# Performance work log

Measured on AMD Instinct MI355X. Metric: run time of the kernel, lower is better.

Reference implementation:

```python
import jax, jax.numpy as jnp
import numpy as np

N_RBF = 20
CUTOFF = 5.0
LN_EPS = 1e-5


def setup_inputs() -> dict:
    key = jax.random.key(0)
    ks = jax.random.split(key, 16)
    N, E, F, H = 20000, 160000, 128, 4
    HF = H * F

    def lin_w(k, fin, fout):
        return (jax.random.normal(k, (fin, fout), jnp.float32) / np.sqrt(fin)).astype(jnp.float32)

    inp = {
        "s_j": jax.random.normal(ks[0], (N, F), jnp.float32),
        "dist": jax.random.uniform(ks[1], (E,), jnp.float32, 0.5, CUTOFF),
        "nbrs": jax.random.randint(ks[2], (E, 2), 0, N),
        # LayerNorm params
        "ln_g": jnp.ones((F,), jnp.float32),
        "ln_b": jnp.zeros((F,), jnp.float32),
        # q/k/v projections: feat_dim -> num_heads*feat_dim
        "Wq": lin_w(ks[3], F, HF), "bq": 0.01 * jax.random.normal(ks[4], (HF,), jnp.float32),
        "Wk": lin_w(ks[5], F, HF), "bk": 0.01 * jax.random.normal(ks[6], (HF,), jnp.float32),
        "Wv": lin_w(ks[7], F, HF), "bv": 0.01 * jax.random.normal(ks[8], (HF,), jnp.float32),
        # RBF -> distance filters dk/dv (Dense with swish activation)
        "dkW": lin_w(ks[9], N_RBF, HF), "dkb": 0.01 * jax.random.normal(ks[10], (HF,), jnp.float32),
        "dvW": lin_w(ks[11], N_RBF, HF), "dvb": 0.01 * jax.random.normal(ks[12], (HF,), jnp.float32),
        # final dense: num_heads*feat_dim -> 3*feat_dim
        "denseW": lin_w(ks[13], HF, 3 * F), "denseb": 0.01 * jax.random.normal(ks[14], (3 * F,), jnp.float32),
    }
    return inp


def reference(s_j, dist, nbrs, ln_g, ln_b, Wq, bq, Wk, bk, Wv, bv, dkW, dkb, dvW, dvb, denseW, denseb):
    F = s_j.shape[-1]
    HF = Wq.shape[-1]
    H = HF // F
    E = dist.shape[0]

    # LayerNorm over feature dim
    mu = s_j.mean(-1, keepdims=True)
    var = ((s_j - mu) ** 2).mean(-1, keepdims=True)
    inp = (s_j - mu) * jax.lax.rsqrt(var + LN_EPS) * ln_g + ln_b  # [N, F]

    # multi-head q/k/v: [N, H, F]
    q = (inp @ Wq + bq).reshape(-1, H, F)
    k = (inp @ Wk + bk).reshape(-1, H, F)
    v = (inp @ Wv + bv).reshape(-1, H, F)

    # Gaussian RBF expansion of distances: [E, n_rbf]
    centers = jnp.linspace(0.0, CUTOFF, N_RBF, dtype=jnp.float32)
    delta = CUTOFF / (N_RBF - 1)
    e_rbf = jnp.exp(-0.5 * ((dist[:, None] - centers) / delta) ** 2)

    # distance filters (Dense + swish): [E, H, F]
    dk = jax.nn.silu(e_rbf @ dkW + dkb).reshape(E, H, F)
    dv = jax.nn.silu(e_rbf @ dvW + dvb).reshape(E, H, F)

    i_idx, j_idx = nbrs[:, 0], nbrs[:, 1]

    # per-edge multi-head attention weight: silu(sum_f q_i * k_j * dk)
    attn = jax.nn.silu(jnp.einsum('ehf,ehf->eh', q[i_idx] * dk, k[j_idx]))  # [E, H]
    env = 0.5 * (jnp.cos(jnp.pi * dist / CUTOFF) + 1.0)  # cosine cutoff envelope [E]

    msg = (attn * env[:, None])[..., None] * v[j_idx] * dv  # [E, H, F]
    out = msg.reshape(E, HF) @ denseW + denseb  # [E, 3F]
    return out.reshape(E, 3, -1)
```

## Files before the change

kernel.cpp:

```cpp
#include <hip/hip_runtime.h>
#include <cstdint>
#include <cstddef>

typedef unsigned short u16;

#define F_DIM   128
#define HF_DIM  512
#define NRBF    20
#define NOUT    384

using bf16x8 = __attribute__((ext_vector_type(8))) __bf16;
using f32x4  = __attribute__((ext_vector_type(4))) float;

__device__ __forceinline__ float bf2f(u16 u){
    union { unsigned int i; float f; } v; v.i = ((unsigned int)u) << 16; return v.f;
}
__device__ __forceinline__ u16 f2bf(float f){
    union { float f; unsigned int i; } v; v.f = f;
    unsigned int x = v.i;
    unsigned int r = x + 0x7fffu + ((x >> 16) & 1u);
    return (u16)(r >> 16);
}
__device__ __forceinline__ float silu(float x){
    return x * __fdividef(1.0f, 1.0f + __expf(-x));
}

__global__ __launch_bounds__(256) void s0_packW(
    const float* __restrict__ dW, u16* __restrict__ Bp)
{
    const int t = blockIdx.x * 256 + threadIdx.x;
    if (t >= 24 * 16 * 64 * 8) return;
    const int j    = t & 7;
    const int lane = (t >> 3) & 63;
    const int ks   = (t >> 9) & 15;
    const int nt   = t >> 13;
    const int k = ks * 32 + ((lane >> 4) << 3) + j;
    const int n = nt * 16 + (lane & 15);
    Bp[t] = f2bf(dW[(size_t)k * NOUT + n]);
}

__global__ __launch_bounds__(128) void s1_ln(
    const float* __restrict__ s_j, const float* __restrict__ ln_g,
    const float* __restrict__ ln_b, float* __restrict__ inp, int N)
{
    __shared__ float ps[2], pss[2];
    const int n = blockIdx.x;
    const int f = threadIdx.x;
    float x = s_j[(size_t)n * F_DIM + f];
    float s = x, ss = x * x;
    #pragma unroll
    for (int o = 1; o < 64; o <<= 1){
        s  += __shfl_xor(s,  o);
        ss += __shfl_xor(ss, o);
    }
    const int wid = f >> 6;
    if ((f & 63) == 0){ ps[wid] = s; pss[wid] = ss; }
    __syncthreads();
    const float S  = ps[0] + ps[1];
    const float SS = pss[0] + pss[1];
    const float mu  = S * (1.f / 128.f);
    const float var = SS * (1.f / 128.f) - mu * mu;
    const float r   = rsqrtf(var + 1e-5f);
    inp[(size_t)n * F_DIM + f] = (x - mu) * r * ln_g[f] + ln_b[f];
}

#define S2_NT 16
__device__ __forceinline__ void s2_mat(
    const float (*a_s)[F_DIM], const float* __restrict__ W,
    const float* __restrict__ b, u16* __restrict__ o, int n0, int c0)
{
    float acc0[S2_NT], acc1[S2_NT];
    const float b0 = b[c0], b1 = b[c0 + 1];
    #pragma unroll
    for (int n = 0; n < S2_NT; n++){ acc0[n] = b0; acc1[n] = b1; }
    for (int k = 0; k < F_DIM; k += 4){
        const float2 w0 = *(const float2*)(W + (size_t)(k+0) * HF_DIM + c0);
        const float2 w1 = *(const float2*)(W + (size_t)(k+1) * HF_DIM + c0);
        const float2 w2 = *(const float2*)(W + (size_t)(k+2) * HF_DIM + c0);
        const float2 w3 = *(const float2*)(W + (size_t)(k+3) * HF_DIM + c0);
        #pragma unroll
        for (int n = 0; n < S2_NT; n++){
            const float4 av = *(const float4*)&a_s[n][k];
            acc0[n] += av.x*w0.x + av.y*w1.x + av.z*w2.x + av.w*w3.x;
            acc1[n] += av.x*w0.y + av.y*w1.y + av.z*w2.y + av.w*w3.y;
        }
    }
    #pragma unroll
    for (int n = 0; n < S2_NT; n++){
        const unsigned int pack =
            (unsigned int)f2bf(acc0[n]) | ((unsigned int)f2bf(acc1[n]) << 16);
        *(unsigned int*)(o + (size_t)(n0 + n) * HF_DIM + c0) = pack;
    }
}

__global__ __launch_bounds__(256) void s2_qkv_t(
    const float* __restrict__ inp,
    const float* __restrict__ Wq, const float* __restrict__ bq,
    const float* __restrict__ Wk, const float* __restrict__ bk,
    const float* __restrict__ Wv, const float* __restrict__ bv,
    u16* __restrict__ qo, u16* __restrict__ ko, u16* __restrict__ vo, int N)
{
    __shared__ float a_s[S2_NT][F_DIM];
    const int tid = threadIdx.x;
    const int n0 = blockIdx.x * S2_NT;
    for (int i = tid; i < S2_NT * F_DIM / 4; i += 256)
        ((float4*)a_s)[i] = ((const float4*)(inp + (size_t)n0 * F_DIM))[i];
    __syncthreads();
    const int c0 = tid * 2;
    s2_mat(a_s, Wq, bq, qo, n0, c0);
    s2_mat(a_s, Wk, bk, ko, n0, c0);
    s2_mat(a_s, Wv, bv, vo, n0, c0);
}

__global__ __launch_bounds__(256) void s3a_edge_msg(
    const float* __restrict__ dist, const int* __restrict__ nbrs,
    const u16* __restrict__ q_ws, const u16* __restrict__ k_ws, const u16* __restrict__ v_ws,
    const float* __restrict__ dkW, const float* __restrict__ dkb,
    const float* __restrict__ dvW, const float* __restrict__ dvb,
    u16* __restrict__ msg_g, int E, int N)
{
    __shared__ float rbf_sh[32][21];
    __shared__ float env_sh[32];
    const int tid = threadIdx.x;
    const int e0 = blockIdx.x * 32;

    if (tid < 32){
        int de = e0 + tid; if (de >= E) de = E - 1;
        float d = dist[de];
        env_sh[tid] = 0.5f * (__cosf(0.62831853071f * d) + 1.0f);
        const float delta = 5.0f / 19.0f;
        const float invd  = 19.0f / 5.0f;
        #pragma unroll
        for (int r = 0; r < NRBF; r++){
            float t = (d - delta * (float)r) * invd;
            rbf_sh[tid][r] = __expf(-0.5f * t * t);
        }
    }
    __syncthreads();

    const int e_l = tid >> 3, sub = tid & 7;
    const int h = sub >> 1, half = sub & 1;
    const int fb = h * F_DIM + half * 64;
    int e = e0 + e_l; if (e >= E) e = E - 1;
    int i_idx = nbrs[2*e + 0];
    int j_idx = nbrs[2*e + 1];
    i_idx = (i_idx < 0) ? 0 : (i_idx >= N ? N-1 : i_idx);
    j_idx = (j_idx < 0) ? 0 : (j_idx >= N ? N-1 : j_idx);
    float rbf[NRBF];
    #pragma unroll
    for (int r = 0; r < NRBF; r++) rbf[r] = rbf_sh[e_l][r];
    const float env = env_sh[e_l];
    const u16* qrow = q_ws + (size_t)i_idx * HF_DIM + fb;
    const u16* krow = k_ws + (size_t)j_idx * HF_DIM + fb;
    const u16* vrow = v_ws + (size_t)j_idx * HF_DIM + fb;
    u16* mrow = msg_g + (size_t)e * HF_DIM + fb;

    float attn = 0.f;
    for (int c = 0; c < 8; c++){
        const int f0 = c * 8;
        uint4 qu = *(const uint4*)(qrow + f0);
        uint4 ku = *(const uint4*)(krow + f0);
        float a8[8];
        #pragma unroll
        for (int j = 0; j < 8; j++) a8[j] = dkb[fb + f0 + j];
        #pragma unroll
        for (int r = 0; r < NRBF; r++){
            const float rv = rbf[r];
            const float* wp = dkW + (size_t)r * HF_DIM + fb + f0;
            #pragma unroll
            for (int j = 0; j < 8; j++) a8[j] += rv * wp[j];
        }
        const u16* qp = (const u16*)&qu;
        const u16* kp = (const u16*)&ku;
        #pragma unroll
        for (int j = 0; j < 8; j++)
            attn += bf2f(qp[j]) * silu(a8[j]) * bf2f(kp[j]);
    }
    attn += __shfl_xor(attn, 1);
    const float scale = silu(attn) * env;

    for (int c = 0; c < 8; c++){
        const int f0 = c * 8;
        uint4 vu = *(const uint4*)(vrow + f0);
        float a8[8];
        #pragma unroll
        for (int j = 0; j < 8; j++) a8[j] = dvb[fb + f0 + j];
        #pragma unroll
        for (int r = 0; r < NRBF; r++){
            const float rv = rbf[r];
            const float* wp = dvW + (size_t)r * HF_DIM + fb + f0;
            #pragma unroll
            for (int j = 0; j < 8; j++) a8[j] += rv * wp[j];
        }
        const u16* vp = (const u16*)&vu;
        u16 ov[8];
        #pragma unroll
        for (int j = 0; j < 8; j++)
            ov[j] = f2bf(scale * bf2f(vp[j]) * silu(a8[j]));
        *(uint4*)(mrow + f0) = *(const uint4*)ov;
    }
}

__global__ __launch_bounds__(512) void s3b_dense(
    const u16* __restrict__ msg_g, const u16* __restrict__ Bp,
    const float* __restrict__ db, float* __restrict__ out, int E)
{
    __shared__ __align__(16) u16 msg_s[32][520];
    const int tid = threadIdx.x;
    const int e0 = blockIdx.x * 32;

    for (int i = tid; i < 32 * 64; i += 512){
        const int row = i >> 6, ch = i & 63;
        int ge = e0 + row; if (ge >= E) ge = E - 1;
        const uint4 d = *(const uint4*)(msg_g + (size_t)ge * HF_DIM + ch * 8);
        *(uint4*)&msg_s[row][ch * 8] = d;
    }
    __syncthreads();

    const int lane = tid & 63;
    const int wave = tid >> 6;
    const int am   = lane & 15;
    const int akb  = (lane >> 4) << 3;
    const int cn   = lane & 15;
    const int cr0  = (lane >> 4) << 2;

    f32x4 acc[2][3];
    #pragma unroll
    for (int nt = 0; nt < 3; nt++){
        const float bias = db[wave * 48 + nt * 16 + cn];
        acc[0][nt] = (f32x4){bias, bias, bias, bias};
        acc[1][nt] = acc[0][nt];
    }

    const u16* bbase = Bp + (size_t)(wave * 3) * (16 * 64 * 8);

    #pragma unroll 4
    for (int ks = 0; ks < 16; ks++){
        const bf16x8 a0 = *(const bf16x8*)&msg_s[am]     [(ks << 5) + akb];
        const bf16x8 a1 = *(const bf16x8*)&msg_s[16 + am][(ks << 5) + akb];
        #pragma unroll
        for (int nt = 0; nt < 3; nt++){
            const bf16x8 b = *(const bf16x8*)(bbase + (((nt * 16 + ks) * 64 + lane) << 3));
            acc[0][nt] = __builtin_amdgcn_mfma_f32_16x16x32_bf16(a0, b, acc[0][nt], 0, 0, 0);
            acc[1][nt] = __builtin_amdgcn_mfma_f32_16x16x32_bf16(a1, b, acc[1][nt], 0, 0, 0);
        }
    }

    #pragma unroll
    for (int mt = 0; mt < 2; mt++){
        #pragma unroll
        for (int r = 0; r < 4; r++){
            const int grow = e0 + mt * 16 + cr0 + r;
            if (grow < E){
                float* op = out + (size_t)grow * NOUT + wave * 48 + cn;
                #pragma unroll
                for (int nt = 0; nt < 3; nt++)
                    op[nt * 16] = acc[mt][nt][r];
            }
        }
    }
}

__global__ __launch_bounds__(256) void s3_fused(
    const float* __restrict__ dist, const int* __restrict__ nbrs,
    const u16* __restrict__ q_ws, const u16* __restrict__ k_ws, const u16* __restrict__ v_ws,
    const float* __restrict__ dkW, const float* __restrict__ dkb,
    const float* __restrict__ dvW, const float* __restrict__ dvb,
    const u16* __restrict__ Bp, const float* __restrict__ db,
    float* __restrict__ out, int E, int N)
{
    __shared__ __align__(16) u16 msg_s[32][520];
    __shared__ float rbf_sh[32][21];
    __shared__ float env_sh[32];
    const int tid = threadIdx.x;
    const int e0 = blockIdx.x * 32;

    if (tid < 32){
        int de = e0 + tid; if (de >= E) de = E - 1;
        float d = dist[de];
        env_sh[tid] = 0.5f * (__cosf(0.62831853071f * d) + 1.0f);
        const float delta = 5.0f / 19.0f;
        const float invd  = 19.0f / 5.0f;
        #pragma unroll
        for (int r = 0; r < NRBF; r++){
            float t = (d - delta * (float)r) * invd;
            rbf_sh[tid][r] = __expf(-0.5f * t * t);
        }
    }
    __syncthreads();
    {
        const int e_l = tid >> 3, sub = tid & 7;
        const int h = sub >> 1, half = sub & 1;
        const int fb = h * F_DIM + half * 64;
        int e = e0 + e_l; if (e >= E) e = E - 1;
        int i_idx = nbrs[2*e + 0];
        int j_idx = nbrs[2*e + 1];
        i_idx = (i_idx < 0) ? 0 : (i_idx >= N ? N-1 : i_idx);
        j_idx = (j_idx < 0) ? 0 : (j_idx >= N ? N-1 : j_idx);
        float rbf[NRBF];
        #pragma unroll
        for (int r = 0; r < NRBF; r++) rbf[r] = rbf_sh[e_l][r];
        const float env = env_sh[e_l];
        const u16* qrow = q_ws + (size_t)i_idx * HF_DIM + fb;
        const u16* krow = k_ws + (size_t)j_idx * HF_DIM + fb;
        const u16* vrow = v_ws + (size_t)j_idx * HF_DIM + fb;

        float attn = 0.f;
        for (int c = 0; c < 8; c++){
            const int f0 = c * 8;
            uint4 qu = *(const uint4*)(qrow + f0);
            uint4 ku = *(const uint4*)(krow + f0);
            float a8[8];
            #pragma unroll
            for (int j = 0; j < 8; j++) a8[j] = dkb[fb + f0 + j];
            #pragma unroll
            for (int r = 0; r < NRBF; r++){
                const float rv = rbf[r];
                const float* wp = dkW + (size_t)r * HF_DIM + fb + f0;
                #pragma unroll
                for (int j = 0; j < 8; j++) a8[j] += rv * wp[j];
            }
            const u16* qp = (const u16*)&qu;
            const u16* kp = (const u16*)&ku;
            #pragma unroll
            for (int j = 0; j < 8; j++)
                attn += bf2f(qp[j]) * silu(a8[j]) * bf2f(kp[j]);
        }
        attn += __shfl_xor(attn, 1);
        const float scale = silu(attn) * env;

        for (int c = 0; c < 8; c++){
            const int f0 = c * 8;
            uint4 vu = *(const uint4*)(vrow + f0);
            float a8[8];
            #pragma unroll
            for (int j = 0; j < 8; j++) a8[j] = dvb[fb + f0 + j];
            #pragma unroll
            for (int r = 0; r < NRBF; r++){
                const float rv = rbf[r];
                const float* wp = dvW + (size_t)r * HF_DIM + fb + f0;
                #pragma unroll
                for (int j = 0; j < 8; j++) a8[j] += rv * wp[j];
            }
            const u16* vp = (const u16*)&vu;
            u16 ov[8];
            #pragma unroll
            for (int j = 0; j < 8; j++)
                ov[j] = f2bf(scale * bf2f(vp[j]) * silu(a8[j]));
            *(uint4*)&msg_s[e_l][fb + f0] = *(const uint4*)ov;
        }
    }
    __syncthreads();
    {
        const int lane = tid & 63;
        const int wave = tid >> 6;
        const int am   = lane & 15;
        const int akb  = (lane >> 4) << 3;
        const int cn   = lane & 15;
        const int cr0  = (lane >> 4) << 2;

        f32x4 acc[2][6];
        #pragma unroll
        for (int nt = 0; nt < 6; nt++){
            const float bias = db[wave * 96 + nt * 16 + cn];
            acc[0][nt] = (f32x4){bias, bias, bias, bias};
            acc[1][nt] = acc[0][nt];
        }
        const u16* bbase = Bp + (size_t)(wave * 6) * (16 * 64 * 8);
        #pragma unroll 4
        for (int ks = 0; ks < 16; ks++){
            const bf16x8 a0 = *(const bf16x8*)&msg_s[am]     [(ks << 5) + akb];
            const bf16x8 a1 = *(const bf16x8*)&msg_s[16 + am][(ks << 5) + akb];
            #pragma unroll
            for (int nt = 0; nt < 6; nt++){
                const bf16x8 b = *(const bf16x8*)(bbase + (((nt * 16 + ks) * 64 + lane) << 3));
                acc[0][nt] = __builtin_amdgcn_mfma_f32_16x16x32_bf16(a0, b, acc[0][nt], 0, 0, 0);
                acc[1][nt] = __builtin_amdgcn_mfma_f32_16x16x32_bf16(a1, b, acc[1][nt], 0, 0, 0);
            }
        }
        #pragma unroll
        for (int mt = 0; mt < 2; mt++){
            #pragma unroll
            for (int r = 0; r < 4; r++){
                const int grow = e0 + mt * 16 + cr0 + r;
                if (grow < E){
                    float* op = out + (size_t)grow * NOUT + wave * 96 + cn;
                    #pragma unroll
                    for (int nt = 0; nt < 6; nt++)
                        op[nt * 16] = acc[mt][nt][r];
                }
            }
        }
    }
}

extern "C" void kernel_launch(void* const* d_in, const int* in_sizes, int n_in,
                              void* d_out, int out_size, void* d_ws, size_t ws_size,
                              hipStream_t stream)
{
    const float* s_j  = (const float*)d_in[0];
    const float* dist = (const float*)d_in[1];
    const int*   nbrs = (const int*)d_in[2];
    const float* ln_g = (const float*)d_in[3];
    const float* ln_b = (const float*)d_in[4];
    const float* Wq   = (const float*)d_in[5];
    const float* bq   = (const float*)d_in[6];
    const float* Wk   = (const float*)d_in[7];
    const float* bk   = (const float*)d_in[8];
    const float* Wv   = (const float*)d_in[9];
    const float* bv   = (const float*)d_in[10];
    const float* dkW  = (const float*)d_in[11];
    const float* dkb  = (const float*)d_in[12];
    const float* dvW  = (const float*)d_in[13];
    const float* dvb  = (const float*)d_in[14];
    const float* dW   = (const float*)d_in[15];
    const float* db   = (const float*)d_in[16];
    const int N = in_sizes[0] / F_DIM;
    const int E = in_sizes[1];
    (void)n_in; (void)out_size;

    char* ws = (char*)d_ws;
    size_t off = 0;
    auto walloc = [&](size_t bytes) -> void* {
        void* p = ws + off;
        off += (bytes + 255) & ~(size_t)255;
        return p;
    };
    float* inp_ws = (float*)walloc((size_t)N * F_DIM * 4);
    u16*   q_ws   = (u16*)walloc((size_t)N * HF_DIM * 2);
    u16*   k_ws   = (u16*)walloc((size_t)N * HF_DIM * 2);
    u16*   v_ws   = (u16*)walloc((size_t)N * HF_DIM * 2);
    u16*   Bp_ws  = (u16*)walloc((size_t)24 * 16 * 64 * 8 * 2);
    const size_t off_base = off;
    u16*   msg_ws = (u16*)walloc((size_t)E * HF_DIM * 2);
    const bool can_split = (ws_size >= off);
    (void)off_base;

    s0_packW<<<768, 256, 0, stream>>>(dW, Bp_ws);
    s1_ln<<<N, 128, 0, stream>>>(s_j, ln_g, ln_b, inp_ws, N);
    s2_qkv_t<<<(N + S2_NT - 1)/S2_NT, 256, 0, stream>>>(
        inp_ws, Wq, bq, Wk, bk, Wv, bv, q_ws, k_ws, v_ws, N);

    if (can_split){
        s3a_edge_msg<<<(E + 31)/32, 256, 0, stream>>>(
            dist, nbrs, q_ws, k_ws, v_ws,
            dkW, dkb, dvW, dvb, msg_ws, E, N);
        s3b_dense<<<(E + 31)/32, 512, 0, stream>>>(
            msg_ws, Bp_ws, db, (float*)d_out, E);
    } else {
        s3_fused<<<(E + 31)/32, 256, 0, stream>>>(
            dist, nbrs, q_ws, k_ws, v_ws,
            dkW, dkb, dvW, dvb, Bp_ws, db, (float*)d_out, E, N);
    }
}
```

Baseline: 2.093 ms.

## Transpose RBF filter weights, hoist gathers, add nontemporal stores in edge kernels

A new pre-pass transposes the dk/dv RBF weight matrices so that each feature's 20 weights are contiguous. The edge-message kernel can then read them per feature instead of striding across rows. All q/k/v row gathers are issued up front before compute to expose memory-level parallelism, and launch bounds now request 2 blocks per CU. The message writes, message reads and final output stores use nontemporal builtins to reduce cache pollution. In exchange, register pressure rises from holding all gathered rows, and one extra small kernel launch is added.

```diff
diff --git a/kernel.cpp b/kernel.cpp
--- a/kernel.cpp
+++ b/kernel.cpp
@@ -11,6 +11,7 @@
 
 using bf16x8 = __attribute__((ext_vector_type(8))) __bf16;
 using f32x4  = __attribute__((ext_vector_type(4))) float;
+using u32x4  = __attribute__((ext_vector_type(4))) unsigned int;
 
 __device__ __forceinline__ float bf2f(u16 u){
     union { unsigned int i; float f; } v; v.i = ((unsigned int)u) << 16; return v.f;
@@ -39,6 +40,17 @@
     Bp[t] = f2bf(dW[(size_t)k * NOUT + n]);
 }
 
+__global__ __launch_bounds__(256) void s0b_packRBF(
+    const float* __restrict__ dkW, const float* __restrict__ dvW,
+    float* __restrict__ dkp, float* __restrict__ dvp)
+{
+    const int t = blockIdx.x * 256 + threadIdx.x;
+    if (t >= HF_DIM * NRBF) return;
+    const int p = t / NRBF, r = t - p * NRBF;
+    dkp[t] = dkW[(size_t)r * HF_DIM + p];
+    dvp[t] = dvW[(size_t)r * HF_DIM + p];
+}
+
 __global__ __launch_bounds__(128) void s1_ln(
     const float* __restrict__ s_j, const float* __restrict__ ln_g,
     const float* __restrict__ ln_b, float* __restrict__ inp, int N)
@@ -112,11 +124,11 @@
     s2_mat(a_s, Wv, bv, vo, n0, c0);
 }
 
-__global__ __launch_bounds__(256) void s3a_edge_msg(
+__global__ __launch_bounds__(256, 2) void s3a_edge_msg(
     const float* __restrict__ dist, const int* __restrict__ nbrs,
     const u16* __restrict__ q_ws, const u16* __restrict__ k_ws, const u16* __restrict__ v_ws,
-    const float* __restrict__ dkW, const float* __restrict__ dkb,
-    const float* __restrict__ dvW, const float* __restrict__ dvb,
+    const float* __restrict__ dkp, const float* __restrict__ dkb,
+    const float* __restrict__ dvp, const float* __restrict__ dvb,
     u16* __restrict__ msg_g, int E, int N)
 {
     __shared__ float rbf_sh[32][21];
@@ -155,23 +167,30 @@
     const u16* vrow = v_ws + (size_t)j_idx * HF_DIM + fb;
     u16* mrow = msg_g + (size_t)e * HF_DIM + fb;
 
+    const float* wkb = dkp + (size_t)fb * NRBF;
+    const float* wvb = dvp + (size_t)fb * NRBF;
+
+    u32x4 qu[8], ku[8];
+    #pragma unroll
+    for (int c = 0; c < 8; c++) qu[c] = *(const u32x4*)(qrow + c * 8);
+    #pragma unroll
+    for (int c = 0; c < 8; c++) ku[c] = *(const u32x4*)(krow + c * 8);
+
     float attn = 0.f;
+    #pragma unroll
     for (int c = 0; c < 8; c++){
         const int f0 = c * 8;
-        uint4 qu = *(const uint4*)(qrow + f0);
-        uint4 ku = *(const uint4*)(krow + f0);
         float a8[8];
         #pragma unroll
         for (int j = 0; j < 8; j++) a8[j] = dkb[fb + f0 + j];
         #pragma unroll
-        for (int r = 0; r < NRBF; r++){
-            const float rv = rbf[r];
-            const float* wp = dkW + (size_t)r * HF_DIM + fb + f0;
-            #pragma unroll
-            for (int j = 0; j < 8; j++) a8[j] += rv * wp[j];
-        }
-        const u16* qp = (const u16*)&qu;
-        const u16* kp = (const u16*)&ku;
+        for (int j = 0; j < 8; j++){
+            const float* wp = wkb + (f0 + j) * NRBF;
+            #pragma unroll
+            for (int r = 0; r < NRBF; r++) a8[j] += rbf[r] * wp[r];
+        }
+        const u16* qp = (const u16*)&qu[c];
+        const u16* kp = (const u16*)&ku[c];
         #pragma unroll
         for (int j = 0; j < 8; j++)
             attn += bf2f(qp[j]) * silu(a8[j]) * bf2f(kp[j]);
@@ -179,25 +198,28 @@
     attn += __shfl_xor(attn, 1);
     const float scale = silu(attn) * env;
 
+    u32x4 vu[8];
+    #pragma unroll
+    for (int c = 0; c < 8; c++) vu[c] = *(const u32x4*)(vrow + c * 8);
+
+    #pragma unroll
     for (int c = 0; c < 8; c++){
         const int f0 = c * 8;
-        uint4 vu = *(const uint4*)(vrow + f0);
         float a8[8];
         #pragma unroll
         for (int j = 0; j < 8; j++) a8[j] = dvb[fb + f0 + j];
         #pragma unroll
-        for (int r = 0; r < NRBF; r++){
-            const float rv = rbf[r];
-            const float* wp = dvW + (size_t)r * HF_DIM + fb + f0;
-            #pragma unroll
-            for (int j = 0; j < 8; j++) a8[j] += rv * wp[j];
-        }
-        const u16* vp = (const u16*)&vu;
+        for (int j = 0; j < 8; j++){
+            const float* wp = wvb + (f0 + j) * NRBF;
+            #pragma unroll
+            for (int r = 0; r < NRBF; r++) a8[j] += rbf[r] * wp[r];
+        }
+        const u16* vp = (const u16*)&vu[c];
         u16 ov[8];
         #pragma unroll
         for (int j = 0; j < 8; j++)
             ov[j] = f2bf(scale * bf2f(vp[j]) * silu(a8[j]));
-        *(uint4*)(mrow + f0) = *(const uint4*)ov;
+        __builtin_nontemporal_store(*(const u32x4*)ov, (u32x4*)(mrow + f0));
     }
 }
 
@@ -212,8 +234,9 @@
     for (int i = tid; i < 32 * 64; i += 512){
         const int row = i >> 6, ch = i & 63;
         int ge = e0 + row; if (ge >= E) ge = E - 1;
-        const uint4 d = *(const uint4*)(msg_g + (size_t)ge * HF_DIM + ch * 8);
-        *(uint4*)&msg_s[row][ch * 8] = d;
+        const u32x4 d = __builtin_nontemporal_load(
+            (const u32x4*)(msg_g + (size_t)ge * HF_DIM + ch * 8));
+        *(u32x4*)&msg_s[row][ch * 8] = d;
     }
     __syncthreads();
 
@@ -255,7 +278,7 @@
                 float* op = out + (size_t)grow * NOUT + wave * 48 + cn;
                 #pragma unroll
                 for (int nt = 0; nt < 3; nt++)
-                    op[nt * 16] = acc[mt][nt][r];
+                    __builtin_nontemporal_store(acc[mt][nt][r], op + nt * 16);
             }
         }
     }
@@ -308,8 +331,8 @@
         float attn = 0.f;
         for (int c = 0; c < 8; c++){
             const int f0 = c * 8;
-            uint4 qu = *(const uint4*)(qrow + f0);
-            uint4 ku = *(const uint4*)(krow + f0);
+            u32x4 qu = *(const u32x4*)(qrow + f0);
+            u32x4 ku = *(const u32x4*)(krow + f0);
             float a8[8];
             #pragma unroll
             for (int j = 0; j < 8; j++) a8[j] = dkb[fb + f0 + j];
@@ -331,7 +354,7 @@
 
         for (int c = 0; c < 8; c++){
             const int f0 = c * 8;
-            uint4 vu = *(const uint4*)(vrow + f0);
+            u32x4 vu = *(const u32x4*)(vrow + f0);
             float a8[8];
             #pragma unroll
             for (int j = 0; j < 8; j++) a8[j] = dvb[fb + f0 + j];
@@ -347,7 +370,7 @@
             #pragma unroll
             for (int j = 0; j < 8; j++)
                 ov[j] = f2bf(scale * bf2f(vp[j]) * silu(a8[j]));
-            *(uint4*)&msg_s[e_l][fb + f0] = *(const uint4*)ov;
+            *(u32x4*)&msg_s[e_l][fb + f0] = *(const u32x4*)ov;
         }
     }
     __syncthreads();
@@ -431,10 +454,10 @@
     u16*   k_ws   = (u16*)walloc((size_t)N * HF_DIM * 2);
     u16*   v_ws   = (u16*)walloc((size_t)N * HF_DIM * 2);
     u16*   Bp_ws  = (u16*)walloc((size_t)24 * 16 * 64 * 8 * 2);
-    const size_t off_base = off;
+    float* dkp_ws = (float*)walloc((size_t)HF_DIM * NRBF * 4);
+    float* dvp_ws = (float*)walloc((size_t)HF_DIM * NRBF * 4);
     u16*   msg_ws = (u16*)walloc((size_t)E * HF_DIM * 2);
     const bool can_split = (ws_size >= off);
-    (void)off_base;
 
     s0_packW<<<768, 256, 0, stream>>>(dW, Bp_ws);
     s1_ln<<<N, 128, 0, stream>>>(s_j, ln_g, ln_b, inp_ws, N);
@@ -442,9 +465,11 @@
         inp_ws, Wq, bq, Wk, bk, Wv, bv, q_ws, k_ws, v_ws, N);
 
     if (can_split){
+        s0b_packRBF<<<(HF_DIM * NRBF + 255)/256, 256, 0, stream>>>(
+            dkW, dvW, dkp_ws, dvp_ws);
         s3a_edge_msg<<<(E + 31)/32, 256, 0, stream>>>(
             dist, nbrs, q_ws, k_ws, v_ws,
-            dkW, dkb, dvW, dvb, msg_ws, E, N);
+            dkp_ws, dkb, dvp_ws, dvb, msg_ws, E, N);
         s3b_dense<<<(E + 31)/32, 512, 0, stream>>>(
             msg_ws, Bp_ws, db, (float*)d_out, E);
     } else {
```

Result: no change. 2.070 ms (-1.1%).
